# Kernel tuning notes

Hardware: AMD Instinct MI355X
Metric: run time of the kernel (lower is better)

Reference implementation:

```python
import jax, jax.numpy as jnp
import numpy as np
from math import sqrt

V, D, H, HD, L, F, P, NL = 32000, 768, 12, 64, 12, 3072, 2048, 2
B, S = 8, 1024
EPS = 1e-5


def setup_inputs() -> dict:
    key = jax.random.key(0)
    ks = jax.random.split(key, 12)
    n = lambda k, sh: (jax.random.normal(k, sh, jnp.float32) * 0.02)
    return {
        'tokens': jax.random.randint(ks[0], (B, S), 0, V, dtype=jnp.int32),
        'tok_emb': n(ks[1], (V, D)),
        'pos_emb': n(ks[2], (P, D)),
        'emb_ln_s': jnp.ones((D,), jnp.float32), 'emb_ln_b': jnp.zeros((D,), jnp.float32),
        'Wq': n(ks[3], (L, H, D, HD)), 'bq': jnp.zeros((L, H, HD), jnp.float32),
        'Wk': n(ks[4], (L, H, D, HD)), 'bk': jnp.zeros((L, H, HD), jnp.float32),
        'Wv': n(ks[5], (L, H, D, HD)), 'bv': jnp.zeros((L, H, HD), jnp.float32),
        'Wo': n(ks[6], (L, D, D)), 'bo': jnp.zeros((L, D), jnp.float32),
        'ln1_s': jnp.ones((L, D), jnp.float32), 'ln1_b': jnp.zeros((L, D), jnp.float32),
        'ln2_s': jnp.ones((L, D), jnp.float32), 'ln2_b': jnp.zeros((L, D), jnp.float32),
        'W1': n(ks[7], (L, D, F)), 'b1': jnp.zeros((L, F), jnp.float32),
        'W2': n(ks[8], (L, F, D)), 'b2': jnp.zeros((L, D), jnp.float32),
        'Wc': n(ks[9], (D, NL)), 'bc': jnp.zeros((NL,), jnp.float32),
    }


def _ln(x, s, b):
    m = jnp.mean(x, -1, keepdims=True)
    v = jnp.mean((x - m) ** 2, -1, keepdims=True)
    return (x - m) * jax.lax.rsqrt(v + EPS) * s + b


def reference(tokens, tok_emb, pos_emb, emb_ln_s, emb_ln_b,
              Wq, bq, Wk, bk, Wv, bv, Wo, bo,
              ln1_s, ln1_b, ln2_s, ln2_b, W1, b1, W2, b2, Wc, bc):
    b, s = tokens.shape
    # embeddings (dropout is eval-mode identity)
    x = tok_emb[tokens] + pos_emb[:s][None, :, :]          # [b, s, D]
    x = _ln(x, emb_ln_s, emb_ln_b)
    scale = 1.0 / sqrt(HD)
    for l in range(L):
        xn = _ln(x, ln1_s[l], ln1_b[l])
        q = jnp.einsum('bsd,hdk->bhsk', xn, Wq[l]) + bq[l][:, None, :]
        k = jnp.einsum('bsd,hdk->bhsk', xn, Wk[l]) + bk[l][:, None, :]
        v = jnp.einsum('bsd,hdk->bhsk', xn, Wv[l]) + bv[l][:, None, :]
        scores = jnp.einsum('bhsk,bhtk->bhst', q, k) * scale   # [b,H,s,s]
        w = jax.nn.softmax(scores, axis=-1)
        o = jnp.einsum('bhst,bhtk->bhsk', w, v)                # [b,H,s,HD]
        o = o.transpose(0, 2, 1, 3).reshape(b, s, D)           # concat heads
        x = x + o @ Wo[l] + bo[l]
        xn = _ln(x, ln2_s[l], ln2_b[l])
        h = jax.nn.gelu(xn @ W1[l] + b1[l], approximate=False)
        x = x + h @ W2[l] + b2[l]
    # CLS token -> classifier (dropout identity)
    return x[:, 0, :] @ Wc + bc                                # [b, NL]
```

## Files before the change

kernel.cpp:

```cpp
#include <hip/hip_runtime.h>
#include <hip/hip_bf16.h>
#include <math.h>

#define B_   8
#define S_   1024
#define D_   768
#define H_   12
#define HD_  64
#define L_   12
#define F_   3072
#define NTOK 8192

typedef __bf16 bf16x8 __attribute__((ext_vector_type(8)));
typedef float  f32x4  __attribute__((ext_vector_type(4)));
typedef unsigned short u16;

static __device__ __forceinline__ unsigned short f2bf_bits(float f) {
    __hip_bfloat16 h = __float2bfloat16(f);
    return __builtin_bit_cast(unsigned short, h);
}
static __device__ __forceinline__ float bf2f(unsigned short u) {
    unsigned int t = ((unsigned int)u) << 16;
    return __builtin_bit_cast(float, t);
}
static __device__ __forceinline__ void gload16(const void* g, void* l) {
    __builtin_amdgcn_global_load_lds(
        (__attribute__((address_space(1))) void*)g,
        (__attribute__((address_space(3))) void*)l, 16, 0, 0);
}

__global__ __launch_bounds__(256)
void prep_layer_kernel(const float* __restrict__ Wq, const float* __restrict__ Wk,
                       const float* __restrict__ Wv, const float* __restrict__ Wo,
                       const float* __restrict__ W1, const float* __restrict__ W2,
                       int l, __hip_bfloat16* __restrict__ wbuf)
{
    const int id = blockIdx.x;
    const float* src; __hip_bfloat16* dst;
    int R, C, r0, c0;
    if (id < 432) {
        int dtile = id % 12, t = id / 12;
        int which = t / 12, h = t % 12;
        src = (which == 0 ? Wq : which == 1 ? Wk : Wv) + (size_t)(l*12 + h) * 768 * 64;
        dst = wbuf + (size_t)(which*768 + h*64) * 768;
        R = 768; C = 64; r0 = dtile * 64; c0 = 0;
    } else if (id < 576) {
        int t = id - 432;
        src = Wo + (size_t)l * 768 * 768;
        dst = wbuf + 1769472;
        R = 768; C = 768; r0 = (t / 12) * 64; c0 = (t % 12) * 64;
    } else if (id < 1152) {
        int t = id - 576;
        src = W1 + (size_t)l * 768 * 3072;
        dst = wbuf + 2359296;
        R = 768; C = 3072; r0 = (t % 12) * 64; c0 = (t / 12) * 64;
    } else {
        int t = id - 1152;
        src = W2 + (size_t)l * 3072 * 768;
        dst = wbuf + 4718592;
        R = 3072; C = 768; r0 = (t / 12) * 64; c0 = (t % 12) * 64;
    }
    __shared__ u16 T[64][68];
    const int t = threadIdx.x;
    const int row = t >> 2, part = t & 3;
#pragma unroll
    for (int j = 0; j < 4; ++j) {
        const int c4 = (part + j*4) * 4;
        float4 v = *(const float4*)(src + (size_t)(r0 + row) * C + c0 + c4);
        T[c4+0][row] = f2bf_bits(v.x);
        T[c4+1][row] = f2bf_bits(v.y);
        T[c4+2][row] = f2bf_bits(v.z);
        T[c4+3][row] = f2bf_bits(v.w);
    }
    __syncthreads();
    const int c = t >> 2;
    u16* drow = (u16*)dst + (size_t)(c0 + c) * R + r0;
#pragma unroll
    for (int j = 0; j < 4; ++j) {
        const int r4 = (part + j*4) * 4;
        ushort4 pk = *(const ushort4*)&T[c][r4];
        *(ushort4*)(drow + r4) = pk;
    }
}

__global__ __launch_bounds__(256)
void prep_bqkv_kernel(const float* __restrict__ bq, const float* __restrict__ bk,
                      const float* __restrict__ bv, float* __restrict__ bqkv)
{
    int i = blockIdx.x * 256 + threadIdx.x;
    int l = i / 2304, c = i % 2304;
    int which = c / 768, hk = c % 768;
    const float* src = which == 0 ? bq : which == 1 ? bk : bv;
    bqkv[i] = src[l*768 + hk];
}

__global__ __launch_bounds__(256)
void embed_ln_kernel(const int* __restrict__ tokens, const float* __restrict__ tok_emb,
                     const float* __restrict__ pos_emb, const float* __restrict__ gam,
                     const float* __restrict__ bet, float* __restrict__ x)
{
    const int row  = blockIdx.x*4 + (threadIdx.x >> 6);
    const int lane = threadIdx.x & 63;
    const int s    = row & (S_-1);
    const int tok  = tokens[row];
    const float* te = tok_emb + (size_t)tok * D_;
    const float* pe = pos_emb + (size_t)s   * D_;
    float v[12]; float s1 = 0.f, s2 = 0.f;
#pragma unroll
    for (int c = 0; c < 3; ++c) {
        const int base = c*256 + lane*4;
        float4 a = *(const float4*)(te + base);
        float4 p = *(const float4*)(pe + base);
        float t0 = a.x+p.x, t1 = a.y+p.y, t2 = a.z+p.z, t3 = a.w+p.w;
        v[c*4+0]=t0; v[c*4+1]=t1; v[c*4+2]=t2; v[c*4+3]=t3;
        s1 += t0+t1+t2+t3;
        s2 += t0*t0 + t1*t1 + t2*t2 + t3*t3;
    }
#pragma unroll
    for (int off = 32; off > 0; off >>= 1) { s1 += __shfl_xor(s1, off); s2 += __shfl_xor(s2, off); }
    const float mean = s1 * (1.f/768.f);
    const float rstd = rsqrtf(s2*(1.f/768.f) - mean*mean + 1e-5f);
    float* xr = x + (size_t)row * D_;
#pragma unroll
    for (int c = 0; c < 3; ++c) {
        const int base = c*256 + lane*4;
        float4 g = *(const float4*)(gam + base);
        float4 bb = *(const float4*)(bet + base);
        float4 o;
        o.x = (v[c*4+0]-mean)*rstd*g.x + bb.x;
        o.y = (v[c*4+1]-mean)*rstd*g.y + bb.y;
        o.z = (v[c*4+2]-mean)*rstd*g.z + bb.z;
        o.w = (v[c*4+3]-mean)*rstd*g.w + bb.w;
        *(float4*)(xr + base) = o;
    }
}

__global__ __launch_bounds__(256)
void ln_kernel(const float* __restrict__ xin, const float* __restrict__ gam,
               const float* __restrict__ bet, __hip_bfloat16* __restrict__ out)
{
    const int row  = blockIdx.x*4 + (threadIdx.x >> 6);
    const int lane = threadIdx.x & 63;
    const float* xr = xin + (size_t)row * D_;
    float v[12]; float s1 = 0.f, s2 = 0.f;
#pragma unroll
    for (int c = 0; c < 3; ++c) {
        float4 t = *(const float4*)(xr + c*256 + lane*4);
        v[c*4+0]=t.x; v[c*4+1]=t.y; v[c*4+2]=t.z; v[c*4+3]=t.w;
        s1 += t.x+t.y+t.z+t.w;
        s2 += t.x*t.x + t.y*t.y + t.z*t.z + t.w*t.w;
    }
#pragma unroll
    for (int off = 32; off > 0; off >>= 1) { s1 += __shfl_xor(s1, off); s2 += __shfl_xor(s2, off); }
    const float mean = s1 * (1.f/768.f);
    const float rstd = rsqrtf(s2*(1.f/768.f) - mean*mean + 1e-5f);
    unsigned short* op = (unsigned short*)out + (size_t)row * D_;
#pragma unroll
    for (int c = 0; c < 3; ++c) {
        const int base = c*256 + lane*4;
        float4 g = *(const float4*)(gam + base);
        float4 bb = *(const float4*)(bet + base);
        ushort4 pk;
        pk.x = f2bf_bits((v[c*4+0]-mean)*rstd*g.x + bb.x);
        pk.y = f2bf_bits((v[c*4+1]-mean)*rstd*g.y + bb.y);
        pk.z = f2bf_bits((v[c*4+2]-mean)*rstd*g.z + bb.z);
        pk.w = f2bf_bits((v[c*4+3]-mean)*rstd*g.w + bb.w);
        *(ushort4*)(op + base) = pk;
    }
}

template<int EPI>
__global__ __launch_bounds__(512, 2)
void gemm256_kernel(const __hip_bfloat16* __restrict__ A,
                    const __hip_bfloat16* __restrict__ Bt,
                    const float* __restrict__ bias,
                    __hip_bfloat16* __restrict__ outb,
                    __hip_bfloat16* __restrict__ outv,
                    int N, int K, int nTiles)
{
    __shared__ __align__(16) char smem[49152];
    char* const As0 = smem;
    char* const As1 = smem + 16384;
    char* const Bs0 = smem + 32768;
    char* const Bs1 = smem + 40960;

    const int tid  = threadIdx.x;
    const int lane = tid & 63;
    const int wid  = tid >> 6;

    const int nwg   = gridDim.x;
    const int chunk = nwg >> 3;
    const int bid   = blockIdx.x;
    const int swz   = (bid & 7) * chunk + (bid >> 3);
    const int m0 = (swz / nTiles) * 256;
    const int n0 = (swz % nTiles) * 128;

    const int l4 = lane >> 2;
    const int sswz = ((lane & 3) ^ ((l4 >> 1) & 3)) * 8;
    const __hip_bfloat16* aSrc = A  + (size_t)(m0 + wid*16 + l4) * K + sswz;
    const __hip_bfloat16* bSrc = Bt + (size_t)(n0 + wid*16 + l4) * K + sswz;
    const int sOff = wid*1024 + lane*16;

    f32x4 acc[4][4] = {};
    const int wm = wid >> 1, wn = wid & 1;
    const int cl = lane & 15, hi = lane >> 4;

    int aoff[4], boff[4];
#pragma unroll
    for (int m = 0; m < 4; ++m) {
        const int row = wm*64 + m*16 + cl;
        aoff[m] = row*64 + ((hi ^ ((row >> 1) & 3)) << 4);
    }
#pragma unroll
    for (int n = 0; n < 4; ++n) {
        const int row = wn*64 + n*16 + cl;
        boff[n] = row*64 + ((hi ^ ((row >> 1) & 3)) << 4);
    }

    auto STAGE = [&](char* aBuf, char* bBuf, int kt) {
        gload16(aSrc + kt,                  aBuf + sOff);
        gload16(aSrc + kt + (size_t)128*K,  aBuf + 8192 + sOff);
        gload16(bSrc + kt,                  bBuf + sOff);
    };

    const int NT = K >> 5;
    STAGE(As0, Bs0, 0);
    STAGE(As1, Bs1, 32);

    for (int t = 0; t < NT; ++t) {
        if (t < NT - 1) asm volatile("s_waitcnt vmcnt(3)" ::: "memory");
        else            asm volatile("s_waitcnt vmcnt(0)" ::: "memory");
        __builtin_amdgcn_s_barrier();

        char* const ac = (t & 1) ? As1 : As0;
        char* const bc = (t & 1) ? Bs1 : Bs0;
        bf16x8 af[4], bfr[4];
#pragma unroll
        for (int m = 0; m < 4; ++m) af[m]  = *(const bf16x8*)(ac + aoff[m]);
#pragma unroll
        for (int n = 0; n < 4; ++n) bfr[n] = *(const bf16x8*)(bc + boff[n]);
        asm volatile("s_waitcnt lgkmcnt(0)" ::: "memory");
        __builtin_amdgcn_sched_barrier(0);
        __builtin_amdgcn_s_barrier();

        if (t + 2 < NT) STAGE(ac, bc, (t + 2) << 5);

        __builtin_amdgcn_s_setprio(1);
#pragma unroll
        for (int m = 0; m < 4; ++m)
#pragma unroll
            for (int n = 0; n < 4; ++n)
                acc[m][n] = __builtin_amdgcn_mfma_f32_16x16x32_bf16(af[m], bfr[n], acc[m][n], 0, 0, 0);
        __builtin_amdgcn_s_setprio(0);
    }

    const bool vpath = (EPI == 0) && (n0 >= 1536);

    if (!vpath) {
        const int strideN = (EPI == 0) ? 1536 : N;
#pragma unroll
        for (int n = 0; n < 4; ++n) {
            const int col = n0 + wn*64 + n*16 + cl;
            const float bv = bias[col];
#pragma unroll
            for (int m = 0; m < 4; ++m) {
#pragma unroll
                for (int i = 0; i < 4; ++i) {
                    const int row = m0 + wm*64 + m*16 + hi*4 + i;
                    float v = acc[m][n][i] + bv;
                    if constexpr (EPI == 1) {
                        const float y = 0.7978845608f * (v + 0.044715f*v*v*v);
                        const float e = __expf(-2.0f * fabsf(y));
                        const float th = (1.0f - e) / (1.0f + e);
                        v = 0.5f * v * (1.0f + copysignf(th, y));
                    }
                    outb[(size_t)row*strideN + col] = __float2bfloat16(v);
                }
            }
        }
    } else {
        const int hdbase = n0 - 1536;
        const int bb = m0 >> 10;
#pragma unroll
        for (int half = 0; half < 2; ++half) {
            __syncthreads();
            if ((wm >> 1) == half) {
#pragma unroll
                for (int n = 0; n < 4; ++n) {
                    const int hdl = wn*64 + n*16 + cl;
                    const float bv = bias[n0 + hdl];
#pragma unroll
                    for (int m = 0; m < 4; ++m) {
                        const int sl = (wm & 1)*64 + m*16 + hi*4;
                        ushort4 pk;
                        pk.x = f2bf_bits(acc[m][n][0] + bv);
                        pk.y = f2bf_bits(acc[m][n][1] + bv);
                        pk.z = f2bf_bits(acc[m][n][2] + bv);
                        pk.w = f2bf_bits(acc[m][n][3] + bv);
                        *(ushort4*)(smem + hdl*256 + ((((sl >> 3) ^ (hdl & 15))) << 4)
                                         + (sl & 7)*2) = pk;
                    }
                }
            }
            __syncthreads();
            const int hdl2 = tid >> 2;
            const int q4   = tid & 3;
            u16* dst = (u16*)outv + ((size_t)(bb*768) + hdbase + hdl2)*1024
                                  + (m0 & 1023) + half*128;
#pragma unroll
            for (int j = 0; j < 4; ++j) {
                const int ch = q4*4 + j;
                const int slot = ch ^ (hdl2 & 15);
                *(float4*)((char*)dst + ch*16) = *(const float4*)(smem + hdl2*256 + (slot << 4));
            }
        }
    }
}

__global__ __launch_bounds__(256)
void gemm_res_kernel(const __hip_bfloat16* __restrict__ A,
                     const __hip_bfloat16* __restrict__ Bt,
                     const float* __restrict__ bias,
                     float* __restrict__ outf,
                     int N, int K, int nTiles)
{
    __shared__ __align__(16) char smem[49152];
    char* const As0 = smem;
    char* const As1 = smem + 8192;
    char* const Bs0 = smem + 16384;
    char* const Bs1 = smem + 32768;

    const int tid  = threadIdx.x;
    const int lane = tid & 63;
    const int wid  = tid >> 6;

    const int nwg   = gridDim.x;
    const int chunk = nwg >> 3;
    const int bid   = blockIdx.x;
    const int swz   = (bid & 7) * chunk + (bid >> 3);
    const int m0 = (swz / nTiles) * 64;
    const int n0 = (swz % nTiles) * 128;

    const int lrow = lane >> 3;
    const int scol = ((lane & 7) ^ lrow) * 8;
    const __hip_bfloat16* aSrc = A  + (size_t)(m0 + wid*16 + lrow) * K + scol;
    const __hip_bfloat16* bSrc = Bt + (size_t)(n0 + wid*32 + lrow) * K + scol;
    const int aOff = wid*2048 + lane*16;
    const int bOff = wid*4096 + lane*16;

    f32x4 acc[2][4] = {};
    const int wm = wid >> 1, wn = wid & 1;
    const int cl = lane & 15, hi = lane >> 4;

    auto STAGE = [&](char* aBuf, char* bBuf, int kt) {
#pragma unroll
        for (int i = 0; i < 2; ++i)
            gload16(aSrc + kt + (size_t)i*8*K, aBuf + aOff + i*1024);
#pragma unroll
        for (int i = 0; i < 4; ++i)
            gload16(bSrc + kt + (size_t)i*8*K, bBuf + bOff + i*1024);
    };

    const int NT = K >> 6;
    STAGE(As0, Bs0, 0);
    STAGE(As1, Bs1, 64);

    for (int t = 0; t < NT; ++t) {
        if (t < NT - 1) asm volatile("s_waitcnt vmcnt(6)" ::: "memory");
        else            asm volatile("s_waitcnt vmcnt(0)" ::: "memory");
        __builtin_amdgcn_s_barrier();

        char* const ac = (t & 1) ? As1 : As0;
        char* const bc = (t & 1) ? Bs1 : Bs0;
        bf16x8 af[2][2], bfr[2][4];
#pragma unroll
        for (int kk = 0; kk < 2; ++kk) {
#pragma unroll
            for (int m = 0; m < 2; ++m) {
                const int row  = wm*32 + m*16 + cl;
                const int slot = ((kk<<2) + hi) ^ (row & 7);
                af[kk][m] = *(const bf16x8*)(ac + row*128 + slot*16);
            }
#pragma unroll
            for (int n = 0; n < 4; ++n) {
                const int row  = wn*64 + n*16 + cl;
                const int slot = ((kk<<2) + hi) ^ (row & 7);
                bfr[kk][n] = *(const bf16x8*)(bc + row*128 + slot*16);
            }
        }
        asm volatile("s_waitcnt lgkmcnt(0)" ::: "memory");
        __builtin_amdgcn_sched_barrier(0);
        __builtin_amdgcn_s_barrier();

        if (t + 2 < NT) STAGE(ac, bc, (t + 2) << 6);

        __builtin_amdgcn_s_setprio(1);
#pragma unroll
        for (int kk = 0; kk < 2; ++kk)
#pragma unroll
            for (int m = 0; m < 2; ++m)
#pragma unroll
                for (int n = 0; n < 4; ++n)
                    acc[m][n] = __builtin_amdgcn_mfma_f32_16x16x32_bf16(af[kk][m], bfr[kk][n], acc[m][n], 0, 0, 0);
        __builtin_amdgcn_s_setprio(0);
    }

    __syncthreads();

#pragma unroll
    for (int n = 0; n < 4; ++n) {
        const int col = wn*64 + n*16 + cl;
        const float bv = bias[n0 + col];
#pragma unroll
        for (int m = 0; m < 2; ++m) {
#pragma unroll
            for (int i = 0; i < 4; ++i) {
                const int row = wm*32 + m*16 + hi*4 + i;
                *(float*)(smem + row*512 + ((((col >> 2) ^ (row & 31))) << 4)
                               + ((col & 3) << 2)) = acc[m][n][i] + bv;
            }
        }
    }
    __syncthreads();
    const int r = tid >> 2;
    const int part = tid & 3;
    float* drow = outf + (size_t)(m0 + r) * N + n0;
#pragma unroll
    for (int j = 0; j < 8; ++j) {
        const int ch = part + j*4;
        f32x4 vv = *(const f32x4*)(smem + r*512 + ((ch ^ (r & 31)) << 4));
        float* dp = drow + ch*4;
        f32x4 g = *(const f32x4*)dp;
        g += vv;
        *(f32x4*)dp = g;
    }
}

__global__ __launch_bounds__(512)
void attn_kernel(const __hip_bfloat16* __restrict__ qkb, const __hip_bfloat16* __restrict__ vtb,
                 __hip_bfloat16* __restrict__ attno)
{
    __shared__ __align__(16) char Ks[2][8192];
    __shared__ __align__(16) char Vs[2][8192];
    __shared__ __align__(16) char Ps[16384];

    const u16* qk = (const u16*)qkb;
    const u16* vt = (const u16*)vtb;
    const int nwg = gridDim.x, bid = blockIdx.x, chunk = nwg >> 3;
    const int swz = (bid & 7) * chunk + (bid >> 3);
    const int bh = swz >> 3, qb = swz & 7;
    const int b = bh / H_, h = bh % H_;
    const int tid = threadIdx.x;
    const int lane = tid & 63, wid = tid >> 6;
    const int cl = lane & 15, hi = lane >> 4;
    const size_t browq = (size_t)(b*S_ + qb*128);

    bf16x8 qf[2];
    {
        const u16* qp = qk + (browq + wid*16 + cl)*1536 + h*64;
        qf[0] = *(const bf16x8*)(qp + hi*8);
        qf[1] = *(const bf16x8*)(qp + 32 + hi*8);
    }

    const int lrow = lane >> 3;
    const int scol = ((lane & 7) ^ lrow) * 8;
    const u16* kbase = qk + ((size_t)b*S_ + wid*8 + lrow)*1536 + 768 + h*64 + scol;
    const u16* vbase = vt + (((size_t)(b*H_ + h))*64 + wid*8 + lrow)*1024 + scol;
    const int ldst = wid*1024 + lane*16;

    f32x4 acc_o[4] = {};
    float m_run = -1e30f;
    float l_part[4] = {0.f, 0.f, 0.f, 0.f};
    char* pbase = Ps + wid*2048;

    {
        gload16(kbase, Ks[0] + ldst);
        gload16(vbase, Vs[0] + ldst);
    }

    for (int t = 0; t < 16; ++t) {
        __syncthreads();
        if (t < 15) {
            const int nb = (t+1) & 1;
            gload16(kbase + (size_t)(t+1)*64*1536, Ks[nb] + ldst);
            gload16(vbase + (t+1)*64,              Vs[nb] + ldst);
        }
        const char* ks = Ks[t & 1];
        const char* vs = Vs[t & 1];

        f32x4 sc[4] = {};
#pragma unroll
        for (int kk = 0; kk < 2; ++kk) {
            bf16x8 kf[4];
#pragma unroll
            for (int n = 0; n < 4; ++n) {
                const int row = n*16 + cl;
                kf[n] = *(const bf16x8*)(ks + row*128 + (((kk*4 + hi) ^ (cl & 7)) << 4));
            }
#pragma unroll
            for (int n = 0; n < 4; ++n)
                sc[n] = __builtin_amdgcn_mfma_f32_16x16x32_bf16(qf[kk], kf[n], sc[n], 0, 0, 0);
        }

#pragma unroll
        for (int n = 0; n < 4; ++n)
#pragma unroll
            for (int i = 0; i < 4; ++i)
                sc[n][i] *= 0.125f;

        float gmax = sc[0][0];
#pragma unroll
        for (int n = 0; n < 4; ++n)
#pragma unroll
            for (int i = 0; i < 4; ++i)
                gmax = fmaxf(gmax, sc[n][i]);
        gmax = fmaxf(gmax, __shfl_xor(gmax, 1));
        gmax = fmaxf(gmax, __shfl_xor(gmax, 2));
        gmax = fmaxf(gmax, __shfl_xor(gmax, 4));
        gmax = fmaxf(gmax, __shfl_xor(gmax, 8));
        if (gmax > m_run + 4.0f) {
            const float corr = __expf(m_run - gmax);
            m_run = gmax;
#pragma unroll
            for (int i = 0; i < 4; ++i) l_part[i] *= corr;
#pragma unroll
            for (int nd = 0; nd < 4; ++nd)
#pragma unroll
                for (int i = 0; i < 4; ++i)
                    acc_o[nd][i] *= corr;
        }

#pragma unroll
        for (int n = 0; n < 4; ++n) {
#pragma unroll
            for (int i = 0; i < 4; ++i) {
                const float e = __expf(sc[n][i] - m_run);
                l_part[i] += e;
                const int q = hi*4 + i;
                const int slot = (n*2 + (cl >> 3)) ^ (q & 7);
                *(u16*)(pbase + q*128 + slot*16 + (cl & 7)*2) = f2bf_bits(e);
            }
        }

        asm volatile("s_waitcnt lgkmcnt(0)" ::: "memory");
        __builtin_amdgcn_sched_barrier(0);

#pragma unroll
        for (int kk = 0; kk < 2; ++kk) {
            const bf16x8 pf = *(const bf16x8*)(pbase + cl*128 + (((kk*4 + hi) ^ (cl & 7)) << 4));
            bf16x8 vf[4];
#pragma unroll
            for (int nd = 0; nd < 4; ++nd) {
                const int d = nd*16 + cl;
                vf[nd] = *(const bf16x8*)(vs + d*128 + (((kk*4 + hi) ^ (d & 7)) << 4));
            }
#pragma unroll
            for (int nd = 0; nd < 4; ++nd)
                acc_o[nd] = __builtin_amdgcn_mfma_f32_16x16x32_bf16(pf, vf[nd], acc_o[nd], 0, 0, 0);
        }
    }

    u16* op = (u16*)attno;
#pragma unroll
    for (int i = 0; i < 4; ++i) {
        float l = l_part[i];
        l += __shfl_xor(l, 1);
        l += __shfl_xor(l, 2);
        l += __shfl_xor(l, 4);
        l += __shfl_xor(l, 8);
        const float inv = 1.f / l;
        const size_t row = browq + wid*16 + hi*4 + i;
#pragma unroll
        for (int nd = 0; nd < 4; ++nd)
            op[row*768 + h*64 + nd*16 + cl] = f2bf_bits(acc_o[nd][i] * inv);
    }
}

__global__ __launch_bounds__(256)
void cls_kernel(const float* __restrict__ x, const float* __restrict__ Wc,
                const float* __restrict__ bc, float* __restrict__ out)
{
    const int b = blockIdx.x;
    const float* xr = x + (size_t)b * S_ * D_;
    float a0 = 0.f, a1 = 0.f;
    for (int d = threadIdx.x; d < 768; d += 256) {
        float xv = xr[d];
        a0 += xv * Wc[d*2+0];
        a1 += xv * Wc[d*2+1];
    }
#pragma unroll
    for (int off = 32; off > 0; off >>= 1) { a0 += __shfl_xor(a0, off); a1 += __shfl_xor(a1, off); }
    __shared__ float r0[4], r1[4];
    const int w = threadIdx.x >> 6;
    if ((threadIdx.x & 63) == 0) { r0[w] = a0; r1[w] = a1; }
    __syncthreads();
    if (threadIdx.x == 0) {
        out[b*2+0] = r0[0]+r0[1]+r0[2]+r0[3] + bc[0];
        out[b*2+1] = r1[0]+r1[1]+r1[2]+r1[3] + bc[1];
    }
}

extern "C" void kernel_launch(void* const* d_in, const int* in_sizes, int n_in,
                              void* d_out, int out_size, void* d_ws, size_t ws_size,
                              hipStream_t stream)
{
    const int*   tokens  = (const int*)  d_in[0];
    const float* tok_emb = (const float*)d_in[1];
    const float* pos_emb = (const float*)d_in[2];
    const float* e_s     = (const float*)d_in[3];
    const float* e_b     = (const float*)d_in[4];
    const float* Wq      = (const float*)d_in[5];
    const float* bq      = (const float*)d_in[6];
    const float* Wk      = (const float*)d_in[7];
    const float* bk      = (const float*)d_in[8];
    const float* Wv      = (const float*)d_in[9];
    const float* bv      = (const float*)d_in[10];
    const float* Wo      = (const float*)d_in[11];
    const float* bo      = (const float*)d_in[12];
    const float* l1s     = (const float*)d_in[13];
    const float* l1b     = (const float*)d_in[14];
    const float* l2s     = (const float*)d_in[15];
    const float* l2b     = (const float*)d_in[16];
    const float* W1      = (const float*)d_in[17];
    const float* b1      = (const float*)d_in[18];
    const float* W2      = (const float*)d_in[19];
    const float* b2      = (const float*)d_in[20];
    const float* Wc      = (const float*)d_in[21];
    const float* bc      = (const float*)d_in[22];
    (void)in_sizes; (void)n_in; (void)out_size;

    if (ws_size < 102346752) return;

    char* ws = (char*)d_ws;
    __hip_bfloat16* wbuf = (__hip_bfloat16*)(ws + 0);
    float*          bqkv = (float*)(ws + 14155776);
    float*          x    = (float*)(ws + 14266368);
    __hip_bfloat16* xn   = (__hip_bfloat16*)(ws + 39432192);
    __hip_bfloat16* qk   = (__hip_bfloat16*)(ws + 52015104);
    __hip_bfloat16* vT   = (__hip_bfloat16*)(ws + 77180928);
    __hip_bfloat16* att  = (__hip_bfloat16*)(ws + 89763840);
    __hip_bfloat16* hbuf = qk;

    __hip_bfloat16* wqkv_t = wbuf;
    __hip_bfloat16* wo_t   = wbuf + 1769472;
    __hip_bfloat16* w1_t   = wbuf + 2359296;
    __hip_bfloat16* w2_t   = wbuf + 4718592;

    prep_bqkv_kernel<<<108, 256, 0, stream>>>(bq, bk, bv, bqkv);
    embed_ln_kernel<<<2048, 256, 0, stream>>>(tokens, tok_emb, pos_emb, e_s, e_b, x);

    for (int l = 0; l < L_; ++l) {
        prep_layer_kernel<<<1728, 256, 0, stream>>>(Wq, Wk, Wv, Wo, W1, W2, l, wbuf);
        ln_kernel<<<2048, 256, 0, stream>>>(x, l1s + l*768, l1b + l*768, xn);
        gemm256_kernel<0><<<576, 512, 0, stream>>>(xn, wqkv_t, bqkv + l*2304, qk, vT, 2304, 768, 18);
        attn_kernel<<<768, 512, 0, stream>>>(qk, vT, att);
        gemm_res_kernel<<<768, 256, 0, stream>>>(att, wo_t, bo + l*768, x, 768, 768, 6);
        ln_kernel<<<2048, 256, 0, stream>>>(x, l2s + l*768, l2b + l*768, xn);
        gemm256_kernel<1><<<768, 512, 0, stream>>>(xn, w1_t, b1 + l*3072, hbuf, nullptr, 3072, 768, 24);
        gemm_res_kernel<<<768, 256, 0, stream>>>(hbuf, w2_t, b2 + l*768, x, 768, 3072, 6);
    }
    cls_kernel<<<8, 256, 0, stream>>>(x, Wc, bc, (float*)d_out);
}
```

Before: 2.949 ms.

## Use 128x128 tiles for residual GEMMs and batch weight prep for all layers

New measurement: 3.048 ms. 3.4% more time.

```diff
diff --git a/kernel.cpp b/kernel.cpp
--- a/kernel.cpp
+++ b/kernel.cpp
@@ -10,6 +10,7 @@
 #define L_   12
 #define F_   3072
 #define NTOK 8192
+#define WBUF_ELEMS 7077888
 
 typedef __bf16 bf16x8 __attribute__((ext_vector_type(8)));
 typedef float  f32x4  __attribute__((ext_vector_type(4)));
@@ -33,31 +34,34 @@
 void prep_layer_kernel(const float* __restrict__ Wq, const float* __restrict__ Wk,
                        const float* __restrict__ Wv, const float* __restrict__ Wo,
                        const float* __restrict__ W1, const float* __restrict__ W2,
-                       int l, __hip_bfloat16* __restrict__ wbuf)
-{
-    const int id = blockIdx.x;
+                       int l0, __hip_bfloat16* __restrict__ wbuf)
+{
+    const int lrel = blockIdx.x / 1728;
+    const int id = blockIdx.x - lrel * 1728;
+    const int l = l0 + lrel;
+    __hip_bfloat16* wb = wbuf + (size_t)lrel * WBUF_ELEMS;
     const float* src; __hip_bfloat16* dst;
     int R, C, r0, c0;
     if (id < 432) {
         int dtile = id % 12, t = id / 12;
         int which = t / 12, h = t % 12;
         src = (which == 0 ? Wq : which == 1 ? Wk : Wv) + (size_t)(l*12 + h) * 768 * 64;
-        dst = wbuf + (size_t)(which*768 + h*64) * 768;
+        dst = wb + (size_t)(which*768 + h*64) * 768;
         R = 768; C = 64; r0 = dtile * 64; c0 = 0;
     } else if (id < 576) {
         int t = id - 432;
         src = Wo + (size_t)l * 768 * 768;
-        dst = wbuf + 1769472;
+        dst = wb + 1769472;
         R = 768; C = 768; r0 = (t / 12) * 64; c0 = (t % 12) * 64;
     } else if (id < 1152) {
         int t = id - 576;
         src = W1 + (size_t)l * 768 * 3072;
-        dst = wbuf + 2359296;
+        dst = wb + 2359296;
         R = 768; C = 3072; r0 = (t % 12) * 64; c0 = (t / 12) * 64;
     } else {
         int t = id - 1152;
         src = W2 + (size_t)l * 3072 * 768;
-        dst = wbuf + 4718592;
+        dst = wb + 4718592;
         R = 3072; C = 768; r0 = (t / 12) * 64; c0 = (t % 12) * 64;
     }
     __shared__ u16 T[64][68];
@@ -317,18 +321,18 @@
     }
 }
 
-__global__ __launch_bounds__(256)
-void gemm_res_kernel(const __hip_bfloat16* __restrict__ A,
-                     const __hip_bfloat16* __restrict__ Bt,
-                     const float* __restrict__ bias,
-                     float* __restrict__ outf,
-                     int N, int K, int nTiles)
-{
-    __shared__ __align__(16) char smem[49152];
+__global__ __launch_bounds__(256, 2)
+void gemm128_res_kernel(const __hip_bfloat16* __restrict__ A,
+                        const __hip_bfloat16* __restrict__ Bt,
+                        const float* __restrict__ bias,
+                        float* __restrict__ outf,
+                        int N, int K, int nTiles)
+{
+    __shared__ __align__(16) char smem[32768];
     char* const As0 = smem;
     char* const As1 = smem + 8192;
     char* const Bs0 = smem + 16384;
-    char* const Bs1 = smem + 32768;
+    char* const Bs1 = smem + 24576;
 
     const int tid  = threadIdx.x;
     const int lane = tid & 63;
@@ -338,101 +342,102 @@
     const int chunk = nwg >> 3;
     const int bid   = blockIdx.x;
     const int swz   = (bid & 7) * chunk + (bid >> 3);
-    const int m0 = (swz / nTiles) * 64;
+    const int m0 = (swz / nTiles) * 128;
     const int n0 = (swz % nTiles) * 128;
 
-    const int lrow = lane >> 3;
-    const int scol = ((lane & 7) ^ lrow) * 8;
-    const __hip_bfloat16* aSrc = A  + (size_t)(m0 + wid*16 + lrow) * K + scol;
-    const __hip_bfloat16* bSrc = Bt + (size_t)(n0 + wid*32 + lrow) * K + scol;
-    const int aOff = wid*2048 + lane*16;
-    const int bOff = wid*4096 + lane*16;
-
-    f32x4 acc[2][4] = {};
+    const int l4 = lane >> 2;
+    const int sswz = ((lane & 3) ^ ((l4 >> 1) & 3)) * 8;
+    const __hip_bfloat16* aSrc = A  + (size_t)(m0 + wid*32 + l4) * K + sswz;
+    const __hip_bfloat16* bSrc = Bt + (size_t)(n0 + wid*32 + l4) * K + sswz;
+    const int sOff = wid*2048 + lane*16;
+
+    f32x4 acc[4][4] = {};
     const int wm = wid >> 1, wn = wid & 1;
     const int cl = lane & 15, hi = lane >> 4;
 
+    int aoff[4], boff[4];
+#pragma unroll
+    for (int m = 0; m < 4; ++m) {
+        const int row = wm*64 + m*16 + cl;
+        aoff[m] = row*64 + ((hi ^ ((row >> 1) & 3)) << 4);
+    }
+#pragma unroll
+    for (int n = 0; n < 4; ++n) {
+        const int row = wn*64 + n*16 + cl;
+        boff[n] = row*64 + ((hi ^ ((row >> 1) & 3)) << 4);
+    }
+
     auto STAGE = [&](char* aBuf, char* bBuf, int kt) {
 #pragma unroll
-        for (int i = 0; i < 2; ++i)
-            gload16(aSrc + kt + (size_t)i*8*K, aBuf + aOff + i*1024);
-#pragma unroll
-        for (int i = 0; i < 4; ++i)
-            gload16(bSrc + kt + (size_t)i*8*K, bBuf + bOff + i*1024);
+        for (int i = 0; i < 2; ++i) {
+            gload16(aSrc + kt + (size_t)i*16*K, aBuf + sOff + i*1024);
+            gload16(bSrc + kt + (size_t)i*16*K, bBuf + sOff + i*1024);
+        }
     };
 
-    const int NT = K >> 6;
+    const int NT = K >> 5;
     STAGE(As0, Bs0, 0);
-    STAGE(As1, Bs1, 64);
+    STAGE(As1, Bs1, 32);
 
     for (int t = 0; t < NT; ++t) {
-        if (t < NT - 1) asm volatile("s_waitcnt vmcnt(6)" ::: "memory");
+        if (t < NT - 1) asm volatile("s_waitcnt vmcnt(4)" ::: "memory");
         else            asm volatile("s_waitcnt vmcnt(0)" ::: "memory");
         __builtin_amdgcn_s_barrier();
 
         char* const ac = (t & 1) ? As1 : As0;
         char* const bc = (t & 1) ? Bs1 : Bs0;
-        bf16x8 af[2][2], bfr[2][4];
-#pragma unroll
-        for (int kk = 0; kk < 2; ++kk) {
-#pragma unroll
-            for (int m = 0; m < 2; ++m) {
-                const int row  = wm*32 + m*16 + cl;
-                const int slot = ((kk<<2) + hi) ^ (row & 7);
-                af[kk][m] = *(const bf16x8*)(ac + row*128 + slot*16);
-            }
-#pragma unroll
-            for (int n = 0; n < 4; ++n) {
-                const int row  = wn*64 + n*16 + cl;
-                const int slot = ((kk<<2) + hi) ^ (row & 7);
-                bfr[kk][n] = *(const bf16x8*)(bc + row*128 + slot*16);
-            }
-        }
+        bf16x8 af[4], bfr[4];
+#pragma unroll
+        for (int m = 0; m < 4; ++m) af[m]  = *(const bf16x8*)(ac + aoff[m]);
+#pragma unroll
+        for (int n = 0; n < 4; ++n) bfr[n] = *(const bf16x8*)(bc + boff[n]);
         asm volatile("s_waitcnt lgkmcnt(0)" ::: "memory");
         __builtin_amdgcn_sched_barrier(0);
         __builtin_amdgcn_s_barrier();
 
-        if (t + 2 < NT) STAGE(ac, bc, (t + 2) << 6);
+        if (t + 2 < NT) STAGE(ac, bc, (t + 2) << 5);
 
         __builtin_amdgcn_s_setprio(1);
 #pragma unroll
-        for (int kk = 0; kk < 2; ++kk)
-#pragma unroll
-            for (int m = 0; m < 2; ++m)
-#pragma unroll
-                for (int n = 0; n < 4; ++n)
-                    acc[m][n] = __builtin_amdgcn_mfma_f32_16x16x32_bf16(af[kk][m], bfr[kk][n], acc[m][n], 0, 0, 0);
+        for (int m = 0; m < 4; ++m)
+#pragma unroll
+            for (int n = 0; n < 4; ++n)
+                acc[m][n] = __builtin_amdgcn_mfma_f32_16x16x32_bf16(af[m], bfr[n], acc[m][n], 0, 0, 0);
         __builtin_amdgcn_s_setprio(0);
     }
 
-    __syncthreads();
-
-#pragma unroll
-    for (int n = 0; n < 4; ++n) {
-        const int col = wn*64 + n*16 + cl;
-        const float bv = bias[n0 + col];
-#pragma unroll
-        for (int m = 0; m < 2; ++m) {
-#pragma unroll
-            for (int i = 0; i < 4; ++i) {
-                const int row = wm*32 + m*16 + hi*4 + i;
-                *(float*)(smem + row*512 + ((((col >> 2) ^ (row & 31))) << 4)
-                               + ((col & 3) << 2)) = acc[m][n][i] + bv;
+#pragma unroll
+    for (int half = 0; half < 2; ++half) {
+        __syncthreads();
+        if (wm == half) {
+#pragma unroll
+            for (int n = 0; n < 4; ++n) {
+                const int col = wn*64 + n*16 + cl;
+                const float bv = bias[n0 + col];
+#pragma unroll
+                for (int m = 0; m < 4; ++m) {
+#pragma unroll
+                    for (int i = 0; i < 4; ++i) {
+                        const int row = m*16 + hi*4 + i;
+                        *(float*)(smem + row*512 + ((((col >> 2) ^ (row & 31))) << 4)
+                                       + ((col & 3) << 2)) = acc[m][n][i] + bv;
+                    }
+                }
             }
         }
-    }
-    __syncthreads();
-    const int r = tid >> 2;
-    const int part = tid & 3;
-    float* drow = outf + (size_t)(m0 + r) * N + n0;
-#pragma unroll
-    for (int j = 0; j < 8; ++j) {
-        const int ch = part + j*4;
-        f32x4 vv = *(const f32x4*)(smem + r*512 + ((ch ^ (r & 31)) << 4));
-        float* dp = drow + ch*4;
-        f32x4 g = *(const f32x4*)dp;
-        g += vv;
-        *(f32x4*)dp = g;
+        __syncthreads();
+        const int r = tid >> 2;
+        const int part = tid & 3;
+        float* drow = outf + (size_t)(m0 + half*64 + r) * N + n0;
+#pragma unroll
+        for (int j = 0; j < 8; ++j) {
+            const int ch = part + j*4;
+            f32x4 vv = *(const f32x4*)(smem + r*512 + ((ch ^ (r & 31)) << 4));
+            float* dp = drow + ch*4;
+            f32x4 g = *(const f32x4*)dp;
+            g += vv;
+            *(f32x4*)dp = g;
+        }
     }
 }
 
@@ -630,34 +635,40 @@
     (void)in_sizes; (void)n_in; (void)out_size;
 
     if (ws_size < 102346752) return;
-
-    char* ws = (char*)d_ws;
-    __hip_bfloat16* wbuf = (__hip_bfloat16*)(ws + 0);
-    float*          bqkv = (float*)(ws + 14155776);
-    float*          x    = (float*)(ws + 14266368);
-    __hip_bfloat16* xn   = (__hip_bfloat16*)(ws + 39432192);
-    __hip_bfloat16* qk   = (__hip_bfloat16*)(ws + 52015104);
-    __hip_bfloat16* vT   = (__hip_bfloat16*)(ws + 77180928);
-    __hip_bfloat16* att  = (__hip_bfloat16*)(ws + 89763840);
+    const bool big = ws_size >= 258060288;
+    const size_t wbufBytes = big ? (size_t)12 * 14155776 : 14155776;
+
+    char* p = (char*)d_ws;
+    __hip_bfloat16* wbuf = (__hip_bfloat16*)p;  p += wbufBytes;
+    float*          bqkv = (float*)p;           p += 110592;
+    float*          x    = (float*)p;           p += 25165824;
+    __hip_bfloat16* xn   = (__hip_bfloat16*)p;  p += 12582912;
+    __hip_bfloat16* qk   = (__hip_bfloat16*)p;  p += 25165824;
+    __hip_bfloat16* vT   = (__hip_bfloat16*)p;  p += 12582912;
+    __hip_bfloat16* att  = (__hip_bfloat16*)p;  p += 12582912;
     __hip_bfloat16* hbuf = qk;
-
-    __hip_bfloat16* wqkv_t = wbuf;
-    __hip_bfloat16* wo_t   = wbuf + 1769472;
-    __hip_bfloat16* w1_t   = wbuf + 2359296;
-    __hip_bfloat16* w2_t   = wbuf + 4718592;
 
     prep_bqkv_kernel<<<108, 256, 0, stream>>>(bq, bk, bv, bqkv);
     embed_ln_kernel<<<2048, 256, 0, stream>>>(tokens, tok_emb, pos_emb, e_s, e_b, x);
+    if (big)
+        prep_layer_kernel<<<1728*12, 256, 0, stream>>>(Wq, Wk, Wv, Wo, W1, W2, 0, wbuf);
 
     for (int l = 0; l < L_; ++l) {
-        prep_layer_kernel<<<1728, 256, 0, stream>>>(Wq, Wk, Wv, Wo, W1, W2, l, wbuf);
+        __hip_bfloat16* wb = wbuf + (big ? (size_t)l * WBUF_ELEMS : 0);
+        __hip_bfloat16* wqkv_t = wb;
+        __hip_bfloat16* wo_t   = wb + 1769472;
+        __hip_bfloat16* w1_t   = wb + 2359296;
+        __hip_bfloat16* w2_t   = wb + 4718592;
+
+        if (!big)
+            prep_layer_kernel<<<1728, 256, 0, stream>>>(Wq, Wk, Wv, Wo, W1, W2, l, wb);
         ln_kernel<<<2048, 256, 0, stream>>>(x, l1s + l*768, l1b + l*768, xn);
         gemm256_kernel<0><<<576, 512, 0, stream>>>(xn, wqkv_t, bqkv + l*2304, qk, vT, 2304, 768, 18);
         attn_kernel<<<768, 512, 0, stream>>>(qk, vT, att);
-        gemm_res_kernel<<<768, 256, 0, stream>>>(att, wo_t, bo + l*768, x, 768, 768, 6);
+        gemm128_res_kernel<<<384, 256, 0, stream>>>(att, wo_t, bo + l*768, x, 768, 768, 6);
         ln_kernel<<<2048, 256, 0, stream>>>(x, l2s + l*768, l2b + l*768, xn);
         gemm256_kernel<1><<<768, 512, 0, stream>>>(xn, w1_t, b1 + l*3072, hbuf, nullptr, 3072, 768, 24);
-        gemm_res_kernel<<<768, 256, 0, stream>>>(hbuf, w2_t, b2 + l*768, x, 768, 3072, 6);
+        gemm128_res_kernel<<<384, 256, 0, stream>>>(hbuf, w2_t, b2 + l*768, x, 768, 3072, 6);
     }
     cls_kernel<<<8, 256, 0, stream>>>(x, Wc, bc, (float*)d_out);
 }
```
